# Kernel optimization log

Measured on AMD Instinct MI355X. Metric: run time of the kernel, lower is better.

Reference implementation:

```python
import jax, jax.numpy as jnp
import numpy as np

BEV_H, BEV_W, ED, HEADS, HD, LEVELS, POINTS, LAYERS = 200, 200, 128, 8, 16, 4, 8, 2
SPATIAL = [(128, 256), (64, 128), (32, 64), (16, 32)]
NV = sum(h * w for h, w in SPATIAL)
NQ = BEV_H * BEV_W
NCLS = 21


def setup_inputs() -> dict:
    key = jax.random.key(0)
    ks = iter(jax.random.split(key, 48))
    r = lambda shape, s=0.02: jax.random.normal(next(ks), shape, jnp.float32) * s
    inp = dict(
        value=r((1, NV, ED), 1.0),
        bev_queries=r((NQ, ED), 0.02),
        bev_pos=r((NQ, ED), 0.02),
        proj_indices=jax.random.randint(next(ks), (1, BEV_H, BEV_W), 0, 250000),
        Wv=r((LAYERS, ED, ED)), bv=jnp.zeros((LAYERS, ED)),
        Woff=r((LAYERS, ED, HEADS * LEVELS * POINTS * 2), 0.01),
        boff=jnp.zeros((LAYERS, HEADS * LEVELS * POINTS * 2)),
        Wattn=r((LAYERS, ED, HEADS * LEVELS * POINTS), 0.01),
        battn=jnp.zeros((LAYERS, HEADS * LEVELS * POINTS)),
        Wout=r((LAYERS, ED, ED)), bout=jnp.zeros((LAYERS, ED)),
        Wf1=r((LAYERS, ED, ED)), bf1=jnp.zeros((LAYERS, ED)),
        Wf2=r((LAYERS, ED, ED)), bf2=jnp.zeros((LAYERS, ED)),
        ln_g=jnp.ones((LAYERS, 2, ED)), ln_b=jnp.zeros((LAYERS, 2, ED)),
        cw1=r((128, ED, 7, 7), 0.01), g1=jnp.ones(128), b1=jnp.zeros(128),
        cw2=r((64, 128, 3, 3), 0.02), g2=jnp.ones(64), b2=jnp.zeros(64),
        cw3=r((48, 64, 3, 3), 0.02), g3=jnp.ones(48), b3=jnp.zeros(48),
        cw4=r((48, 48, 3, 3), 0.02), g4=jnp.ones(48), b4=jnp.zeros(48),
        objw=r((NCLS, 48, 1, 1), 0.05), objb=jnp.zeros(NCLS),
    )
    return inp


def _ln(x, g, b):
    m = x.mean(-1, keepdims=True)
    v = ((x - m) ** 2).mean(-1, keepdims=True)
    return (x - m) * jax.lax.rsqrt(v + 1e-5) * g + b


def _deform_attn(q, value, Wv, bv, Woff, boff, Wattn, battn, Wout, bout, ref):
    # multi-scale deformable attention (Deformable-DETR / BEVFormer core)
    v = (value[0] @ Wv + bv).reshape(NV, HEADS, HD)
    off = (q @ Woff + boff).reshape(NQ, HEADS, LEVELS, POINTS, 2)
    attn = jax.nn.softmax((q @ Wattn + battn).reshape(NQ, HEADS, LEVELS * POINTS), -1)
    attn = attn.reshape(NQ, HEADS, LEVELS, POINTS)
    out = jnp.zeros((HEADS, NQ, HD), jnp.float32)
    start = 0
    for l, (H, W) in enumerate(SPATIAL):
        vl = v[start:start + H * W].transpose(1, 0, 2)  # [HEADS, H*W, HD]
        start += H * W
        # normalized sampling locations in [0,1]
        loc = ref[:, None, None, :] + off[:, :, l] / jnp.array([W, H], jnp.float32)
        x = loc[..., 0] * W - 0.5  # grid_sample align_corners=False convention
        y = loc[..., 1] * H - 0.5  # [NQ, HEADS, POINTS]
        x0 = jnp.floor(x)
        y0 = jnp.floor(y)
        acc = jnp.zeros((HEADS, NQ, POINTS, HD), jnp.float32)
        for dx, dy in ((0, 0), (1, 0), (0, 1), (1, 1)):
            xc = x0 + dx
            yc = y0 + dy
            wgt = (1.0 - jnp.abs(x - xc)) * (1.0 - jnp.abs(y - yc))
            valid = (xc >= 0) & (xc < W) & (yc >= 0) & (yc < H)
            xi = jnp.clip(xc, 0, W - 1).astype(jnp.int32)
            yi = jnp.clip(yc, 0, H - 1).astype(jnp.int32)
            idx = (yi * W + xi).transpose(1, 0, 2)  # [HEADS, NQ, POINTS]
            g = jax.vmap(lambda vh, ih: vh[ih])(vl, idx)  # [HEADS, NQ, POINTS, HD]
            acc = acc + (wgt * valid).transpose(1, 0, 2)[..., None] * g
        out = out + jnp.einsum('nhp,hnpd->hnd', attn[:, :, l], acc)
    return out.transpose(1, 0, 2).reshape(NQ, ED) @ Wout + bout


def _bev_encoder(bev_queries, bev_pos, value, Wv, bv, Woff, boff, Wattn, battn, Wout, bout, Wf1, bf1, Wf2, bf2, ln_g, ln_b):
    gx = (jnp.arange(BEV_W, dtype=jnp.float32) + 0.5) / BEV_W
    gy = (jnp.arange(BEV_H, dtype=jnp.float32) + 0.5) / BEV_H
    ref = jnp.stack(jnp.meshgrid(gx, gy), -1).reshape(NQ, 2)  # (x, y)
    q = bev_queries
    for i in range(LAYERS):  # operation_order: cross_attn, norm, ffn, norm
        a = _deform_attn(q + bev_pos, value, Wv[i], bv[i], Woff[i], boff[i],
                         Wattn[i], battn[i], Wout[i], bout[i], ref)
        q = _ln(q + a, ln_g[i, 0], ln_b[i, 0])
        h = jax.nn.relu(q @ Wf1[i] + bf1[i]) @ Wf2[i] + bf2[i]
        q = _ln(q + h, ln_g[i, 1], ln_b[i, 1])
    return q


def _conv(x, w, p):
    return jax.lax.conv_general_dilated(x, w, (1, 1), [(p, p), (p, p)],
                                        dimension_numbers=('NCHW', 'OIHW', 'NCHW'))


def _bn_relu(x, g, b):
    m = x.mean((0, 2, 3), keepdims=True)
    v = x.var((0, 2, 3), keepdims=True)
    return jax.nn.relu((x - m) * jax.lax.rsqrt(v + 1e-5) * g[None, :, None, None] + b[None, :, None, None])


def reference(value, bev_queries, bev_pos, proj_indices, Wv, bv, Woff, boff, Wattn, battn, Wout, bout, Wf1, bf1, Wf2, bf2, ln_g, ln_b, cw1, g1, b1, cw2, g2, b2, cw3, g3, b3, cw4, g4, b4, objw, objb):
    observed_masks = proj_indices < jnp.max(proj_indices)  # mask_update
    q = _bev_encoder(bev_queries, bev_pos, value, Wv, bv, Woff, boff, Wattn, battn,
                     Wout, bout, Wf1, bf1, Wf2, bf2, ln_g, ln_b)
    mem = q.reshape(1, BEV_H, BEV_W, ED).transpose(0, 3, 1, 2)  # [1, ED, H, W]
    h = _bn_relu(_conv(mem, cw1, 3), g1, b1)
    h = _bn_relu(_conv(h, cw2, 1), g2, b2)
    h = _bn_relu(_conv(h, cw3, 1), g3, b3)
    h = _bn_relu(_conv(h, cw4, 1), g4, b4)
    semmap = _conv(h, objw, 0) + objb[None, :, None, None]
    return semmap, observed_masks
```

## Files before the change

kernel.cpp:

```cpp
#include <hip/hip_runtime.h>
#include <cstdint>
#include <cstddef>

#define NQ 40000
#define EDIM 128
#define NVAL 43520
#define NCLS 21

typedef unsigned short u16;
typedef unsigned int uint;
typedef short bf16x8 __attribute__((ext_vector_type(8)));
typedef float f32x4 __attribute__((ext_vector_type(4)));

__device__ inline u16 f2b(float f) {
    unsigned u = __float_as_uint(f);
    unsigned r = u + 0x7FFF + ((u >> 16) & 1);
    return (u16)(r >> 16);
}
__device__ inline float b2f(u16 v) {
    unsigned u = ((unsigned)v) << 16;
    return __uint_as_float(u);
}
__device__ inline float blo(uint u) { return __uint_as_float(u << 16); }
__device__ inline float bhi(uint u) { return __uint_as_float(u & 0xFFFF0000u); }

__global__ void reduce_max_int(const int* __restrict__ idx, int* __restrict__ mx) {
    int i = blockIdx.x * 256 + threadIdx.x;
    int v = (i < NQ) ? idx[i] : 0;
    for (int o = 32; o > 0; o >>= 1) v = max(v, __shfl_xor(v, o, 64));
    if ((threadIdx.x & 63) == 0) atomicMax(mx, v);
}

__global__ void write_mask(const int* __restrict__ idx, const int* __restrict__ mx,
                           float* __restrict__ out) {
    int i = blockIdx.x * 256 + threadIdx.x;
    if (i >= NQ) return;
    out[i] = (idx[i] < *mx) ? 1.0f : 0.0f;
}

__global__ void cvt_b_k(const float* __restrict__ src, u16* __restrict__ dst, int n8) {
    int i = blockIdx.x * 256 + threadIdx.x;
    if (i >= n8) return;
    const float4 a = ((const float4*)src)[i * 2];
    const float4 b = ((const float4*)src)[i * 2 + 1];
    u16 o[8] = {f2b(a.x), f2b(a.y), f2b(a.z), f2b(a.w), f2b(b.x), f2b(b.y), f2b(b.z), f2b(b.w)};
    ((uint4*)dst)[i] = *(const uint4*)o;
}

__global__ void add2b_k(const float* __restrict__ a, const float* __restrict__ b,
                        u16* __restrict__ c, int n8) {
    int i = blockIdx.x * 256 + threadIdx.x;
    if (i >= n8) return;
    const float4 a0 = ((const float4*)a)[i * 2], a1 = ((const float4*)a)[i * 2 + 1];
    const float4 b0 = ((const float4*)b)[i * 2], b1 = ((const float4*)b)[i * 2 + 1];
    u16 o[8] = {f2b(a0.x + b0.x), f2b(a0.y + b0.y), f2b(a0.z + b0.z), f2b(a0.w + b0.w),
                f2b(a1.x + b1.x), f2b(a1.y + b1.y), f2b(a1.z + b1.z), f2b(a1.w + b1.w)};
    ((uint4*)c)[i] = *(const uint4*)o;
}

__global__ void pack_enc_k(const float* __restrict__ Wv, const float* __restrict__ Woff,
                           const float* __restrict__ Wattn, const float* __restrict__ Wout,
                           const float* __restrict__ Wf1, const float* __restrict__ Wf2,
                           u16* __restrict__ dst) {
    int i = blockIdx.x * 256 + threadIdx.x;
    if (i >= 327680) return;
    int l = i / 163840, r = i % 163840;
    int k = r / 1280, col = r % 1280;
    const float* src; int N; int n; u16* d;
    u16* base = dst + (size_t)l * 163840;
    if (col < 128)       { src = Wv    + (size_t)l * 16384; N = 128; n = col;        d = base;          }
    else if (col < 640)  { src = Woff  + (size_t)l * 65536; N = 512; n = col - 128;  d = base + 16384;  }
    else if (col < 896)  { src = Wattn + (size_t)l * 32768; N = 256; n = col - 640;  d = base + 81920;  }
    else if (col < 1024) { src = Wout  + (size_t)l * 16384; N = 128; n = col - 896;  d = base + 114688; }
    else if (col < 1152) { src = Wf1   + (size_t)l * 16384; N = 128; n = col - 1024; d = base + 131072; }
    else                 { src = Wf2   + (size_t)l * 16384; N = 128; n = col - 1152; d = base + 147456; }
    d[(size_t)n * 128 + k] = f2b(src[(size_t)k * N + n]);
}

__global__ void pack_bias_k(const float* __restrict__ boff, const float* __restrict__ battn,
                            float* __restrict__ dst) {
    int i = blockIdx.x * 256 + threadIdx.x;
    if (i >= 1536) return;
    int l = i / 768, r = i % 768;
    dst[i] = (r < 512) ? boff[(size_t)l * 512 + r] : battn[(size_t)l * 256 + r - 512];
}

__global__ void pack_cw_k(const float* __restrict__ w, u16* __restrict__ wT,
                          int OC, int IC, int KS, int OCp, int ICp) {
    int i = blockIdx.x * 256 + threadIdx.x;
    int tot = KS * KS * OCp * ICp;
    if (i >= tot) return;
    int ic = i % ICp; int r = i / ICp;
    int oc = r % OCp; int tap = r / OCp;
    int ky = tap / KS, kx = tap % KS;
    float v = 0.f;
    if (oc < OC && ic < IC)
        v = w[(((size_t)oc * IC + ic) * KS + ky) * KS + kx];
    wT[i] = f2b(v);
}

__global__ __launch_bounds__(256) void gemm_mfma_k(
        const u16* __restrict__ A, const u16* __restrict__ BT,
        const float* __restrict__ bias, float* __restrict__ Cf,
        u16* __restrict__ Cb, int N, int relu) {
    __shared__ u16 As[64 * 136];
    __shared__ u16 Bs[64 * 136];
    const int m0 = blockIdx.x * 64, n0 = blockIdx.y * 64;
    const int t = threadIdx.x;
#pragma unroll
    for (int ci = t; ci < 1024; ci += 256) {
        int r = ci >> 4, c = ci & 15;
        *(uint4*)&As[r * 136 + c * 8] = *(const uint4*)&A[(size_t)(m0 + r) * 128 + c * 8];
        *(uint4*)&Bs[r * 136 + c * 8] = *(const uint4*)&BT[(size_t)(n0 + r) * 128 + c * 8];
    }
    __syncthreads();
    const int wave = t >> 6, lane = t & 63;
    const int wm = (wave & 1) * 32, wn = (wave >> 1) * 32;
    const int lr = lane & 15, lk = (lane >> 4) * 8;
    f32x4 acc[2][2] = {};
#pragma unroll
    for (int ks = 0; ks < 4; ks++) {
        bf16x8 a0 = *(const bf16x8*)&As[(wm + lr) * 136 + ks * 32 + lk];
        bf16x8 a1 = *(const bf16x8*)&As[(wm + 16 + lr) * 136 + ks * 32 + lk];
        bf16x8 b0 = *(const bf16x8*)&Bs[(wn + lr) * 136 + ks * 32 + lk];
        bf16x8 b1 = *(const bf16x8*)&Bs[(wn + 16 + lr) * 136 + ks * 32 + lk];
        acc[0][0] = __builtin_amdgcn_mfma_f32_16x16x32_bf16(a0, b0, acc[0][0], 0, 0, 0);
        acc[0][1] = __builtin_amdgcn_mfma_f32_16x16x32_bf16(a0, b1, acc[0][1], 0, 0, 0);
        acc[1][0] = __builtin_amdgcn_mfma_f32_16x16x32_bf16(a1, b0, acc[1][0], 0, 0, 0);
        acc[1][1] = __builtin_amdgcn_mfma_f32_16x16x32_bf16(a1, b1, acc[1][1], 0, 0, 0);
    }
    float bj0 = bias[n0 + wn + lr];
    float bj1 = bias[n0 + wn + 16 + lr];
#pragma unroll
    for (int i = 0; i < 2; i++) {
#pragma unroll
        for (int j = 0; j < 2; j++) {
            float bb = j ? bj1 : bj0;
#pragma unroll
            for (int r = 0; r < 4; r++) {
                int ml = wm + i * 16 + (lane >> 4) * 4 + r;
                int nl = wn + j * 16 + lr;
                float v = acc[i][j][r] + bb;
                if (relu) v = fmaxf(v, 0.f);
                size_t o = (size_t)(m0 + ml) * N + n0 + nl;
                if (Cf) Cf[o] = v;
                if (Cb) Cb[o] = f2b(v);
            }
        }
    }
}

template <int KS, int ICP>
__global__ __launch_bounds__(256) void conv5_mfma_k(
        const u16* __restrict__ pimg, const u16* __restrict__ wT,
        float* __restrict__ out, int OCtot) {
    constexpr int PAD = KS / 2;
    constexpr int WIN = 64 + KS - 1;
    constexpr int STR = ICP + 8;
    constexpr int KSTEPS = ICP / 32;
    constexpr int NTAP = KS * KS;
    constexpr int ACH = WIN * (ICP / 8);
    constexpr int NB = ICP / 32;
    __shared__ u16 As[2 * WIN * STR];
    __shared__ u16 Bs[2 * 64 * STR];
    const int bx = blockIdx.x;
    const int yp = (bx >> 2) * 2;
    const int xc = bx & 3;
    const int x0 = (xc == 3) ? 136 : xc * 64;
    const int n0 = blockIdx.y * 64;
    const int t = threadIdx.x;
    const int wave = t >> 6, lane = t & 63;
    const int row = wave >> 1;
    const int wn = (wave & 1) * 32;
    const int lr = lane & 15, lkq = lane >> 4, lk = lkq * 8;

    f32x4 acc[4][2] = {};
    const u16* wbase = wT + (size_t)n0 * ICP;

    uint4 breg[NB];
    int bro[NB], bco[NB];
#pragma unroll
    for (int k = 0; k < NB; k++) {
        int ci = t + k * 256;
        bro[k] = ci / (ICP / 8);
        bco[k] = ci - bro[k] * (ICP / 8);
    }
#pragma unroll
    for (int k = 0; k < NB; k++)
        breg[k] = *(const uint4*)&wbase[(size_t)bro[k] * ICP + bco[k] * 8];
#pragma unroll
    for (int k = 0; k < NB; k++)
        *(uint4*)&Bs[(size_t)bro[k] * STR + bco[k] * 8] = breg[k];

    for (int ky = 0; ky < KS; ky++) {
        __syncthreads();
        {
            const u16* s0 = pimg + (((size_t)(yp + ky + 3 - PAD)) * 208 + (x0 + 3 - PAD)) * ICP;
            const u16* s1 = pimg + (((size_t)(yp + 1 + ky + 3 - PAD)) * 208 + (x0 + 3 - PAD)) * ICP;
            for (int ci = t; ci < 2 * ACH; ci += 256) {
                int w2 = ci / ACH, rem = ci - w2 * ACH;
                int r = rem / (ICP / 8), c = rem - r * (ICP / 8);
                const u16* s = w2 ? s1 : s0;
                *(uint4*)&As[(size_t)(w2 * WIN + r) * STR + c * 8] =
                    *(const uint4*)&s[(size_t)r * ICP + c * 8];
            }
        }
        for (int kx = 0; kx < KS; kx++) {
            const int tap = ky * KS + kx;
            __syncthreads();
            if (tap + 1 < NTAP) {
                const u16* ws = wbase + (size_t)(tap + 1) * OCtot * ICP;
#pragma unroll
                for (int k = 0; k < NB; k++)
                    breg[k] = *(const uint4*)&ws[(size_t)bro[k] * ICP + bco[k] * 8];
            }
            const u16* ab = &As[((size_t)row * WIN + kx) * STR];
            const u16* bb = &Bs[(size_t)((tap & 1) * 64 + wn) * STR];
#pragma unroll
            for (int ks = 0; ks < KSTEPS; ks++) {
                bf16x8 b0 = *(const bf16x8*)&bb[(size_t)lr * STR + ks * 32 + lk];
                bf16x8 b1 = *(const bf16x8*)&bb[(size_t)(lr + 16) * STR + ks * 32 + lk];
#pragma unroll
                for (int i = 0; i < 4; i++) {
                    bf16x8 a = *(const bf16x8*)&ab[(size_t)(lr + i * 16) * STR + ks * 32 + lk];
                    acc[i][0] = __builtin_amdgcn_mfma_f32_16x16x32_bf16(a, b0, acc[i][0], 0, 0, 0);
                    acc[i][1] = __builtin_amdgcn_mfma_f32_16x16x32_bf16(a, b1, acc[i][1], 0, 0, 0);
                }
            }
            if (tap + 1 < NTAP) {
                u16* bd = &Bs[(size_t)(((tap + 1) & 1) * 64) * STR];
#pragma unroll
                for (int k = 0; k < NB; k++)
                    *(uint4*)&bd[(size_t)bro[k] * STR + bco[k] * 8] = breg[k];
            }
        }
    }
    const int px0 = (yp + row) * 200 + x0;
#pragma unroll
    for (int i = 0; i < 4; i++) {
#pragma unroll
        for (int j = 0; j < 2; j++) {
#pragma unroll
            for (int r = 0; r < 4; r++) {
                int ml = i * 16 + lkq * 4 + r;
                int nl = wn + j * 16 + lr;
                out[(size_t)(px0 + ml) * OCtot + n0 + nl] = acc[i][j][r];
            }
        }
    }
}

__global__ __launch_bounds__(256) void deform3_k(
        const u16* __restrict__ v, const u16* __restrict__ oa,
        u16* __restrict__ outb, int q0, int nq) {
    const int t = threadIdx.x;
    const int wq = t >> 6;
    const int lane = t & 63;
    const int s = lane >> 5;
    const int l32 = lane & 31;
    const int h = l32 >> 2;
    const int cl = l32 & 3;
    const int qi = blockIdx.x * 8 + wq * 2 + s;
    if (qi >= nq) return;
    const int gq = q0 + qi;
    const float rx = ((gq % 200) + 0.5f) / 200.f;
    const float ry = ((gq / 200) + 0.5f) / 200.f;

    const uint* lp = (const uint*)(oa + (size_t)qi * 768 + 512 + h * 32);
    float lg[32];
#pragma unroll
    for (int i = 0; i < 16; i++) { uint u = lp[i]; lg[2 * i] = blo(u); lg[2 * i + 1] = bhi(u); }
    float mx = -1e30f;
#pragma unroll
    for (int i = 0; i < 32; i++) mx = fmaxf(mx, lg[i]);
    float ssum = 0.f;
#pragma unroll
    for (int i = 0; i < 32; i++) { lg[i] = __expf(lg[i] - mx); ssum += lg[i]; }
    const float inv = 1.f / ssum;

    const uint* op = (const uint*)(oa + (size_t)qi * 768 + h * 64);

    const int HS[4] = {128, 64, 32, 16};
    const int WS[4] = {256, 128, 64, 32};
    const int ST[4] = {0, 32768, 40960, 43008};
    float a0 = 0.f, a1 = 0.f, a2 = 0.f, a3 = 0.f;
#pragma unroll
    for (int l = 0; l < 4; l++) {
        const int H = HS[l], W = WS[l];
        const float fW = (float)W, fH = (float)H;
        const u16* vb = v + (size_t)ST[l] * 128 + h * 16 + cl * 4;
#pragma unroll
        for (int p = 0; p < 8; p++) {
            uint pr = op[l * 8 + p];
            float ox = blo(pr), oy = bhi(pr);
            float xx = rx * fW + ox - 0.5f;
            float yy = ry * fH + oy - 0.5f;
            float xf = floorf(xx), yf = floorf(yy);
            int ix = (int)xf, iy = (int)yf;
            float fx = xx - xf, fy = yy - yf;
            float aw = lg[l * 8 + p] * inv;
            int x1 = ix + 1, y1 = iy + 1;
            bool vx0 = (unsigned)ix < (unsigned)W;
            bool vx1 = (unsigned)x1 < (unsigned)W;
            bool vy0 = (unsigned)iy < (unsigned)H;
            bool vy1 = (unsigned)y1 < (unsigned)H;
            int cx0 = min(max(ix, 0), W - 1), cx1 = min(max(x1, 0), W - 1);
            int cy0 = min(max(iy, 0), H - 1), cy1 = min(max(y1, 0), H - 1);
            float w00 = (vx0 && vy0) ? (1.f - fx) * (1.f - fy) * aw : 0.f;
            float w10 = (vx1 && vy0) ? fx * (1.f - fy) * aw : 0.f;
            float w01 = (vx0 && vy1) ? (1.f - fx) * fy * aw : 0.f;
            float w11 = (vx1 && vy1) ? fx * fy * aw : 0.f;
            uint2 u00 = *(const uint2*)(vb + (size_t)(cy0 * W + cx0) * 128);
            uint2 u10 = *(const uint2*)(vb + (size_t)(cy0 * W + cx1) * 128);
            uint2 u01 = *(const uint2*)(vb + (size_t)(cy1 * W + cx0) * 128);
            uint2 u11 = *(const uint2*)(vb + (size_t)(cy1 * W + cx1) * 128);
            a0 = fmaf(w00, blo(u00.x), a0); a1 = fmaf(w00, bhi(u00.x), a1);
            a2 = fmaf(w00, blo(u00.y), a2); a3 = fmaf(w00, bhi(u00.y), a3);
            a0 = fmaf(w10, blo(u10.x), a0); a1 = fmaf(w10, bhi(u10.x), a1);
            a2 = fmaf(w10, blo(u10.y), a2); a3 = fmaf(w10, bhi(u10.y), a3);
            a0 = fmaf(w01, blo(u01.x), a0); a1 = fmaf(w01, bhi(u01.x), a1);
            a2 = fmaf(w01, blo(u01.y), a2); a3 = fmaf(w01, bhi(u01.y), a3);
            a0 = fmaf(w11, blo(u11.x), a0); a1 = fmaf(w11, bhi(u11.x), a1);
            a2 = fmaf(w11, blo(u11.y), a2); a3 = fmaf(w11, bhi(u11.y), a3);
        }
    }
    uint2 o;
    o.x = (uint)f2b(a0) | ((uint)f2b(a1) << 16);
    o.y = (uint)f2b(a2) | ((uint)f2b(a3) << 16);
    *(uint2*)(outb + (size_t)gq * 128 + h * 16 + cl * 4) = o;
}

__global__ __launch_bounds__(256) void add_ln_k(
        float* __restrict__ q, const float* __restrict__ a,
        const float* __restrict__ g, const float* __restrict__ b,
        u16* __restrict__ qb) {
    const int row = blockIdx.x * 4 + (threadIdx.x >> 6);
    const int lane = threadIdx.x & 63;
    float s0 = q[(size_t)row * 128 + lane] + a[(size_t)row * 128 + lane];
    float s1 = q[(size_t)row * 128 + 64 + lane] + a[(size_t)row * 128 + 64 + lane];
    float sum = s0 + s1;
    for (int o = 32; o > 0; o >>= 1) sum += __shfl_xor(sum, o, 64);
    float mean = sum * (1.f / 128.f);
    float d0 = s0 - mean, d1 = s1 - mean;
    float vs = d0 * d0 + d1 * d1;
    for (int o = 32; o > 0; o >>= 1) vs += __shfl_xor(vs, o, 64);
    float inv = rsqrtf(vs * (1.f / 128.f) + 1e-5f);
    float o0 = d0 * inv * g[lane] + b[lane];
    float o1 = d1 * inv * g[64 + lane] + b[64 + lane];
    q[(size_t)row * 128 + lane] = o0;
    q[(size_t)row * 128 + 64 + lane] = o1;
    qb[(size_t)row * 128 + lane] = f2b(o0);
    qb[(size_t)row * 128 + 64 + lane] = f2b(o1);
}

__global__ void fill_pimg2_k(const u16* __restrict__ qb, u16* __restrict__ pimg) {
    int i = blockIdx.x * 256 + threadIdx.x;
    if (i >= 685568) return;
    int pp = i >> 4, c8 = i & 15;
    int py = pp / 208, px = pp - py * 208;
    uint4 val = {0u, 0u, 0u, 0u};
    if (py >= 3 && py < 203 && px >= 3 && px < 203)
        val = ((const uint4*)qb)[((size_t)((py - 3) * 200 + (px - 3))) * 16 + c8];
    ((uint4*)pimg)[i] = val;
}

__global__ __launch_bounds__(256) void bn_stats2_k(const float* __restrict__ x,
                                                   float* __restrict__ acc,
                                                   int cSh, int ppb) {
    const int t = threadIdx.x;
    const int Cp = 1 << cSh;
    const int c = t & (Cp - 1);
    const int sub = t >> cSh;
    const int nsub = 256 >> cSh;
    float s = 0.f, s2 = 0.f;
    const int pbase = blockIdx.x * ppb;
    for (int i = sub; i < ppb; i += nsub) {
        float v = x[(size_t)(pbase + i) * Cp + c];
        s += v; s2 += v * v;
    }
    __shared__ float ls[256], ls2[256];
    ls[t] = s; ls2[t] = s2;
    __syncthreads();
    if (t < Cp) {
        for (int k = 1; k < nsub; k++) { s += ls[t + k * Cp]; s2 += ls2[t + k * Cp]; }
        atomicAdd(&acc[2 * t], s);
        atomicAdd(&acc[2 * t + 1], s2);
    }
}

__global__ void bn_fin_k(const float* __restrict__ acc, float* __restrict__ mv, int C) {
    int t = threadIdx.x;
    if (t >= C) return;
    float m = acc[2 * t] * (1.f / 40000.f);
    float var = acc[2 * t + 1] * (1.f / 40000.f) - m * m;
    mv[2 * t] = m;
    mv[2 * t + 1] = rsqrtf(var + 1e-5f);
}

__global__ void bn_apply_pad2_k(const float* __restrict__ x, const float* __restrict__ mv,
                                const float* __restrict__ g, const float* __restrict__ b,
                                u16* __restrict__ outp, int cSh, int Creal) {
    int i = blockIdx.x * 256 + threadIdx.x;
    int Cp = 1 << cSh;
    if (i >= 206 * 208 * Cp) return;
    int c = i & (Cp - 1);
    int pp = i >> cSh;
    int py = pp / 208, px = pp - py * 208;
    float v = 0.f;
    if (c < Creal && py >= 3 && py < 203 && px >= 3 && px < 203) {
        int p = (py - 3) * 200 + (px - 3);
        v = fmaxf((x[(size_t)p * Cp + c] - mv[2 * c]) * mv[2 * c + 1] * g[c] + b[c], 0.f);
    }
    outp[i] = f2b(v);
}

__global__ void bn_apply2_k(const float* __restrict__ x, const float* __restrict__ mv,
                            const float* __restrict__ g, const float* __restrict__ b,
                            u16* __restrict__ outb, int cSh, int Creal) {
    int i = blockIdx.x * 256 + threadIdx.x;
    int Cp = 1 << cSh;
    if (i >= 40000 * Cp) return;
    int c = i & (Cp - 1);
    float v = 0.f;
    if (c < Creal) v = fmaxf((x[i] - mv[2 * c]) * mv[2 * c + 1] * g[c] + b[c], 0.f);
    outb[i] = f2b(v);
}

__global__ void obj_conv_k(const u16* __restrict__ in, const float* __restrict__ w,
                           const float* __restrict__ bias, float* __restrict__ out) {
    int p = blockIdx.x * 256 + threadIdx.x;
    if (p >= 40000) return;
    float xin[48];
#pragma unroll
    for (int c = 0; c < 48; c++) xin[c] = b2f(in[(size_t)p * 64 + c]);
    for (int o = 0; o < NCLS; o++) {
        float acc = bias[o];
#pragma unroll
        for (int c = 0; c < 48; c++) acc += xin[c] * w[o * 48 + c];
        out[(size_t)o * 40000 + p] = acc;
    }
}

extern "C" void kernel_launch(void* const* d_in, const int* in_sizes, int n_in,
                              void* d_out, int out_size, void* d_ws, size_t ws_size,
                              hipStream_t stream) {
    const float* value   = (const float*)d_in[0];
    const float* bev_q   = (const float*)d_in[1];
    const float* bev_pos = (const float*)d_in[2];
    const int*   proj    = (const int*)d_in[3];
    const float* Wv      = (const float*)d_in[4];
    const float* bv      = (const float*)d_in[5];
    const float* Woff    = (const float*)d_in[6];
    const float* boff    = (const float*)d_in[7];
    const float* Wattn   = (const float*)d_in[8];
    const float* battn   = (const float*)d_in[9];
    const float* Wout    = (const float*)d_in[10];
    const float* bout    = (const float*)d_in[11];
    const float* Wf1     = (const float*)d_in[12];
    const float* bf1     = (const float*)d_in[13];
    const float* Wf2     = (const float*)d_in[14];
    const float* bf2     = (const float*)d_in[15];
    const float* ln_g    = (const float*)d_in[16];
    const float* ln_b    = (const float*)d_in[17];
    const float* cw1     = (const float*)d_in[18];
    const float* g1      = (const float*)d_in[19];
    const float* b1      = (const float*)d_in[20];
    const float* cw2     = (const float*)d_in[21];
    const float* g2      = (const float*)d_in[22];
    const float* b2      = (const float*)d_in[23];
    const float* cw3     = (const float*)d_in[24];
    const float* g3      = (const float*)d_in[25];
    const float* b3      = (const float*)d_in[26];
    const float* cw4     = (const float*)d_in[27];
    const float* g4      = (const float*)d_in[28];
    const float* b4      = (const float*)d_in[29];
    const float* objw    = (const float*)d_in[30];
    const float* objb    = (const float*)d_in[31];
    float* out = (float*)d_out;

    float* WSb = (float*)d_ws;
    float* q     = WSb + 0;
    u16*   qb    = (u16*)(WSb + 5120000);
    u16*   qpb   = (u16*)(WSb + 7680000);
    u16*   valb  = (u16*)(WSb + 10240000);
    u16*   vbufb = (u16*)(WSb + 13025280);
    u16*   fb    = (u16*)(WSb + 15810560);
    float* tmp   = WSb + 18882560;
    u16*   aob   = (u16*)(WSb + 24002560);
    u16*   hb    = (u16*)(WSb + 26562560);
    u16*   wenc  = (u16*)(WSb + 29122560);
    u16*   wcv   = (u16*)(WSb + 29286400);
    float* bnacc = WSb + 29761536;
    float* bnmv  = WSb + 29762048;
    int*   maxi  = (int*)(WSb + 29762304);
    float* fbias = WSb + 29762308;

    u16*   pimg = (u16*)(WSb + 10240000);
    float* c1f  = tmp;
    u16*   c1b  = (u16*)(WSb + 13025280);
    float* c2f  = WSb + 0;
    u16*   c2b  = (u16*)(WSb + 5120000);
    float* c3f  = WSb + 2560000;
    u16*   c3b  = (u16*)(WSb + 7680000);
    float* c4f  = WSb + 0;
    u16*   c4b  = (u16*)(WSb + 15810560);

    const size_t L = 163840;
    u16* WvT[2]; u16* WoffT[2]; u16* WoutT[2]; u16* Wf1T[2]; u16* Wf2T[2];
    for (int l = 0; l < 2; l++) {
        u16* base = wenc + l * L;
        WvT[l]    = base;
        WoffT[l]  = base + 16384;
        WoutT[l]  = base + 114688;
        Wf1T[l]   = base + 131072;
        Wf2T[l]   = base + 147456;
    }
    u16* w1T = wcv;
    u16* w2T = wcv + 802816;
    u16* w3T = wcv + 876544;
    u16* w4T = wcv + 913408;

    hipMemsetAsync(maxi, 0, sizeof(int), stream);
    reduce_max_int<<<157, 256, 0, stream>>>(proj, maxi);
    write_mask<<<157, 256, 0, stream>>>(proj, maxi, out + 840000);

    pack_enc_k<<<1280, 256, 0, stream>>>(Wv, Woff, Wattn, Wout, Wf1, Wf2, wenc);
    pack_bias_k<<<6, 256, 0, stream>>>(boff, battn, fbias);
    pack_cw_k<<<3136, 256, 0, stream>>>(cw1, w1T, 128, 128, 7, 128, 128);
    pack_cw_k<<<288, 256, 0, stream>>>(cw2, w2T, 64, 128, 3, 64, 128);
    pack_cw_k<<<144, 256, 0, stream>>>(cw3, w3T, 48, 64, 3, 64, 64);
    pack_cw_k<<<144, 256, 0, stream>>>(cw4, w4T, 48, 48, 3, 64, 64);
    cvt_b_k<<<2720, 256, 0, stream>>>(value, valb, NVAL * 128 / 8);

    hipMemcpyAsync(q, bev_q, (size_t)NQ * EDIM * sizeof(float),
                   hipMemcpyDeviceToDevice, stream);
    const int CH0 = 19968, CH1 = 20032;
    for (int l = 0; l < 2; l++) {
        gemm_mfma_k<<<dim3(680, 2), 256, 0, stream>>>(
            valb, WvT[l], bv + (size_t)l * 128, nullptr, vbufb, 128, 0);
        add2b_k<<<2500, 256, 0, stream>>>(q, bev_pos, qpb, NQ * 128 / 8);
        for (int cidx = 0; cidx < 2; cidx++) {
            int qs = cidx ? CH0 : 0;
            int nq = cidx ? CH1 : CH0;
            gemm_mfma_k<<<dim3(nq / 64, 12), 256, 0, stream>>>(
                qpb + (size_t)qs * 128, WoffT[l], fbias + (size_t)l * 768,
                nullptr, fb, 768, 0);
            deform3_k<<<nq / 8, 256, 0, stream>>>(vbufb, fb, aob, qs, nq);
        }
        gemm_mfma_k<<<dim3(625, 2), 256, 0, stream>>>(
            aob, WoutT[l], bout + (size_t)l * 128, tmp, nullptr, 128, 0);
        add_ln_k<<<10000, 256, 0, stream>>>(q, tmp, ln_g + (size_t)(l * 2 + 0) * 128,
                                            ln_b + (size_t)(l * 2 + 0) * 128, qb);
        gemm_mfma_k<<<dim3(625, 2), 256, 0, stream>>>(
            qb, Wf1T[l], bf1 + (size_t)l * 128, nullptr, hb, 128, 1);
        gemm_mfma_k<<<dim3(625, 2), 256, 0, stream>>>(
            hb, Wf2T[l], bf2 + (size_t)l * 128, tmp, nullptr, 128, 0);
        add_ln_k<<<10000, 256, 0, stream>>>(q, tmp, ln_g + (size_t)(l * 2 + 1) * 128,
                                            ln_b + (size_t)(l * 2 + 1) * 128, qb);
    }

    fill_pimg2_k<<<2678, 256, 0, stream>>>(qb, pimg);

    conv5_mfma_k<7, 128><<<dim3(400, 2), 256, 0, stream>>>(pimg, w1T, c1f, 128);
    hipMemsetAsync(bnacc, 0, 512 * sizeof(float), stream);
    bn_stats2_k<<<125, 256, 0, stream>>>(c1f, bnacc, 7, 320);
    bn_fin_k<<<1, 128, 0, stream>>>(bnacc, bnmv, 128);
    bn_apply_pad2_k<<<21424, 256, 0, stream>>>(c1f, bnmv, g1, b1, c1b, 7, 128);

    conv5_mfma_k<3, 128><<<dim3(400, 1), 256, 0, stream>>>(c1b, w2T, c2f, 64);
    hipMemsetAsync(bnacc, 0, 512 * sizeof(float), stream);
    bn_stats2_k<<<125, 256, 0, stream>>>(c2f, bnacc, 6, 320);
    bn_fin_k<<<1, 64, 0, stream>>>(bnacc, bnmv, 64);
    bn_apply_pad2_k<<<10712, 256, 0, stream>>>(c2f, bnmv, g2, b2, c2b, 6, 64);

    conv5_mfma_k<3, 64><<<dim3(400, 1), 256, 0, stream>>>(c2b, w3T, c3f, 64);
    hipMemsetAsync(bnacc, 0, 512 * sizeof(float), stream);
    bn_stats2_k<<<125, 256, 0, stream>>>(c3f, bnacc, 6, 320);
    bn_fin_k<<<1, 48, 0, stream>>>(bnacc, bnmv, 48);
    bn_apply_pad2_k<<<10712, 256, 0, stream>>>(c3f, bnmv, g3, b3, c3b, 6, 48);

    conv5_mfma_k<3, 64><<<dim3(400, 1), 256, 0, stream>>>(c3b, w4T, c4f, 64);
    hipMemsetAsync(bnacc, 0, 512 * sizeof(float), stream);
    bn_stats2_k<<<125, 256, 0, stream>>>(c4f, bnacc, 6, 320);
    bn_fin_k<<<1, 48, 0, stream>>>(bnacc, bnmv, 48);
    bn_apply2_k<<<10000, 256, 0, stream>>>(c4f, bnmv, g4, b4, c4b, 6, 48);

    obj_conv_k<<<157, 256, 0, stream>>>(c4b, objw, objb, out);
}
```

Measured before the change: 1.024 ms.

## Head-major padded value layout, A-tile reuse in GEMMs, fused BN stats into conv

```diff
diff --git a/kernel.cpp b/kernel.cpp
--- a/kernel.cpp
+++ b/kernel.cpp
@@ -99,159 +99,217 @@
     wT[i] = f2b(v);
 }
 
-__global__ __launch_bounds__(256) void gemm_mfma_k(
+__global__ __launch_bounds__(256) void gemm2_mfma_k(
         const u16* __restrict__ A, const u16* __restrict__ BT,
         const float* __restrict__ bias, float* __restrict__ Cf,
-        u16* __restrict__ Cb, int N, int relu) {
+        u16* __restrict__ Cb, int N, int relu, int NSUB) {
     __shared__ u16 As[64 * 136];
     __shared__ u16 Bs[64 * 136];
-    const int m0 = blockIdx.x * 64, n0 = blockIdx.y * 64;
+    const int m0 = blockIdx.x * 64;
+    const int nbase = blockIdx.y * 64 * NSUB;
     const int t = threadIdx.x;
-#pragma unroll
-    for (int ci = t; ci < 1024; ci += 256) {
-        int r = ci >> 4, c = ci & 15;
-        *(uint4*)&As[r * 136 + c * 8] = *(const uint4*)&A[(size_t)(m0 + r) * 128 + c * 8];
-        *(uint4*)&Bs[r * 136 + c * 8] = *(const uint4*)&BT[(size_t)(n0 + r) * 128 + c * 8];
-    }
-    __syncthreads();
     const int wave = t >> 6, lane = t & 63;
     const int wm = (wave & 1) * 32, wn = (wave >> 1) * 32;
-    const int lr = lane & 15, lk = (lane >> 4) * 8;
-    f32x4 acc[2][2] = {};
-#pragma unroll
-    for (int ks = 0; ks < 4; ks++) {
-        bf16x8 a0 = *(const bf16x8*)&As[(wm + lr) * 136 + ks * 32 + lk];
-        bf16x8 a1 = *(const bf16x8*)&As[(wm + 16 + lr) * 136 + ks * 32 + lk];
-        bf16x8 b0 = *(const bf16x8*)&Bs[(wn + lr) * 136 + ks * 32 + lk];
-        bf16x8 b1 = *(const bf16x8*)&Bs[(wn + 16 + lr) * 136 + ks * 32 + lk];
-        acc[0][0] = __builtin_amdgcn_mfma_f32_16x16x32_bf16(a0, b0, acc[0][0], 0, 0, 0);
-        acc[0][1] = __builtin_amdgcn_mfma_f32_16x16x32_bf16(a0, b1, acc[0][1], 0, 0, 0);
-        acc[1][0] = __builtin_amdgcn_mfma_f32_16x16x32_bf16(a1, b0, acc[1][0], 0, 0, 0);
-        acc[1][1] = __builtin_amdgcn_mfma_f32_16x16x32_bf16(a1, b1, acc[1][1], 0, 0, 0);
-    }
-    float bj0 = bias[n0 + wn + lr];
-    float bj1 = bias[n0 + wn + 16 + lr];
-#pragma unroll
-    for (int i = 0; i < 2; i++) {
-#pragma unroll
-        for (int j = 0; j < 2; j++) {
-            float bb = j ? bj1 : bj0;
+    const int lr = lane & 15, lkq = lane >> 4, lk = lkq * 8;
+    for (int s = 0; s < NSUB; s++) {
+        const int n0 = nbase + s * 64;
+        if (s) __syncthreads();
+#pragma unroll
+        for (int ci = t; ci < 1024; ci += 256) {
+            int r = ci >> 4, c = (ci & 15) * 8;
+            if (s == 0)
+                *(uint4*)&As[r * 136 + c] = *(const uint4*)&A[(size_t)(m0 + r) * 128 + c];
+            *(uint4*)&Bs[r * 136 + c] = *(const uint4*)&BT[(size_t)(n0 + r) * 128 + c];
+        }
+        __syncthreads();
+        f32x4 acc[2][2] = {};
+#pragma unroll
+        for (int ks = 0; ks < 4; ks++) {
+            bf16x8 a0 = *(const bf16x8*)&As[(wm + lr) * 136 + ks * 32 + lk];
+            bf16x8 a1 = *(const bf16x8*)&As[(wm + 16 + lr) * 136 + ks * 32 + lk];
+            bf16x8 b0 = *(const bf16x8*)&Bs[(wn + lr) * 136 + ks * 32 + lk];
+            bf16x8 b1 = *(const bf16x8*)&Bs[(wn + 16 + lr) * 136 + ks * 32 + lk];
+            acc[0][0] = __builtin_amdgcn_mfma_f32_16x16x32_bf16(a0, b0, acc[0][0], 0, 0, 0);
+            acc[0][1] = __builtin_amdgcn_mfma_f32_16x16x32_bf16(a0, b1, acc[0][1], 0, 0, 0);
+            acc[1][0] = __builtin_amdgcn_mfma_f32_16x16x32_bf16(a1, b0, acc[1][0], 0, 0, 0);
+            acc[1][1] = __builtin_amdgcn_mfma_f32_16x16x32_bf16(a1, b1, acc[1][1], 0, 0, 0);
+        }
+        float bj0 = bias[n0 + wn + lr];
+        float bj1 = bias[n0 + wn + 16 + lr];
+#pragma unroll
+        for (int i = 0; i < 2; i++) {
+#pragma unroll
+            for (int j = 0; j < 2; j++) {
+                float bb = j ? bj1 : bj0;
+#pragma unroll
+                for (int r = 0; r < 4; r++) {
+                    int ml = wm + i * 16 + lkq * 4 + r;
+                    int nl = wn + j * 16 + lr;
+                    float v = acc[i][j][r] + bb;
+                    if (relu) v = fmaxf(v, 0.f);
+                    size_t o = (size_t)(m0 + ml) * N + n0 + nl;
+                    if (Cf) Cf[o] = v;
+                    if (Cb) Cb[o] = f2b(v);
+                }
+            }
+        }
+    }
+}
+
+__global__ __launch_bounds__(256) void gemm_vh_k(
+        const u16* __restrict__ A, const u16* __restrict__ BT,
+        const float* __restrict__ bias, u16* __restrict__ vh) {
+    __shared__ u16 As[64 * 136];
+    __shared__ u16 Bs[64 * 136];
+    const int m0 = blockIdx.x * 64;
+    const int t = threadIdx.x;
+    const int wave = t >> 6, lane = t & 63;
+    const int wm = (wave & 1) * 32, wn = (wave >> 1) * 32;
+    const int lr = lane & 15, lkq = lane >> 4, lk = lkq * 8;
+    for (int s = 0; s < 2; s++) {
+        const int n0 = s * 64;
+        if (s) __syncthreads();
+#pragma unroll
+        for (int ci = t; ci < 1024; ci += 256) {
+            int r = ci >> 4, c = (ci & 15) * 8;
+            if (s == 0)
+                *(uint4*)&As[r * 136 + c] = *(const uint4*)&A[(size_t)(m0 + r) * 128 + c];
+            *(uint4*)&Bs[r * 136 + c] = *(const uint4*)&BT[(size_t)(n0 + r) * 128 + c];
+        }
+        __syncthreads();
+        f32x4 acc[2][2] = {};
+#pragma unroll
+        for (int ks = 0; ks < 4; ks++) {
+            bf16x8 a0 = *(const bf16x8*)&As[(wm + lr) * 136 + ks * 32 + lk];
+            bf16x8 a1 = *(const bf16x8*)&As[(wm + 16 + lr) * 136 + ks * 32 + lk];
+            bf16x8 b0 = *(const bf16x8*)&Bs[(wn + lr) * 136 + ks * 32 + lk];
+            bf16x8 b1 = *(const bf16x8*)&Bs[(wn + 16 + lr) * 136 + ks * 32 + lk];
+            acc[0][0] = __builtin_amdgcn_mfma_f32_16x16x32_bf16(a0, b0, acc[0][0], 0, 0, 0);
+            acc[0][1] = __builtin_amdgcn_mfma_f32_16x16x32_bf16(a0, b1, acc[0][1], 0, 0, 0);
+            acc[1][0] = __builtin_amdgcn_mfma_f32_16x16x32_bf16(a1, b0, acc[1][0], 0, 0, 0);
+            acc[1][1] = __builtin_amdgcn_mfma_f32_16x16x32_bf16(a1, b1, acc[1][1], 0, 0, 0);
+        }
+        float bj0 = bias[n0 + wn + lr];
+        float bj1 = bias[n0 + wn + 16 + lr];
+#pragma unroll
+        for (int i = 0; i < 2; i++) {
 #pragma unroll
             for (int r = 0; r < 4; r++) {
-                int ml = wm + i * 16 + (lane >> 4) * 4 + r;
-                int nl = wn + j * 16 + lr;
-                float v = acc[i][j][r] + bb;
-                if (relu) v = fmaxf(v, 0.f);
-                size_t o = (size_t)(m0 + ml) * N + n0 + nl;
-                if (Cf) Cf[o] = v;
-                if (Cb) Cb[o] = f2b(v);
+                int p = m0 + wm + i * 16 + lkq * 4 + r;
+                int idx;
+                if (p < 32768)      idx = (p >> 8) * 257 + (p & 255);
+                else if (p < 40960) { int pp = p - 32768; idx = 32896 + (pp >> 7) * 129 + (pp & 127); }
+                else if (p < 43008) { int pp = p - 40960; idx = 41152 + (pp >> 6) * 65 + (pp & 63); }
+                else                { int pp = p - 43008; idx = 43232 + (pp >> 5) * 33 + (pp & 31); }
+#pragma unroll
+                for (int j = 0; j < 2; j++) {
+                    int c = n0 + wn + j * 16 + lr;
+                    float v = acc[i][j][r] + (j ? bj1 : bj0);
+                    vh[((size_t)(c >> 4) * 43760 + idx) * 16 + (c & 15)] = f2b(v);
+                }
             }
         }
     }
 }
 
 template <int KS, int ICP>
-__global__ __launch_bounds__(256) void conv5_mfma_k(
+__global__ __launch_bounds__(256) void conv6_mfma_k(
         const u16* __restrict__ pimg, const u16* __restrict__ wT,
-        float* __restrict__ out, int OCtot) {
+        float* __restrict__ out, float* __restrict__ bnacc, int OCtot) {
     constexpr int PAD = KS / 2;
-    constexpr int WIN = 64 + KS - 1;
     constexpr int STR = ICP + 8;
+    constexpr int NTAP = KS * KS;
     constexpr int KSTEPS = ICP / 32;
-    constexpr int NTAP = KS * KS;
-    constexpr int ACH = WIN * (ICP / 8);
     constexpr int NB = ICP / 32;
-    __shared__ u16 As[2 * WIN * STR];
     __shared__ u16 Bs[2 * 64 * STR];
     const int bx = blockIdx.x;
-    const int yp = (bx >> 2) * 2;
+    const int y = bx >> 2;
     const int xc = bx & 3;
     const int x0 = (xc == 3) ? 136 : xc * 64;
     const int n0 = blockIdx.y * 64;
     const int t = threadIdx.x;
     const int wave = t >> 6, lane = t & 63;
-    const int row = wave >> 1;
-    const int wn = (wave & 1) * 32;
+    const int wm = (wave & 1) * 32, wn = (wave >> 1) * 32;
     const int lr = lane & 15, lkq = lane >> 4, lk = lkq * 8;
 
-    f32x4 acc[4][2] = {};
-    const u16* wbase = wT + (size_t)n0 * ICP;
-
-    uint4 breg[NB];
+    f32x4 acc[2][2] = {};
     int bro[NB], bco[NB];
 #pragma unroll
     for (int k = 0; k < NB; k++) {
         int ci = t + k * 256;
         bro[k] = ci / (ICP / 8);
-        bco[k] = ci - bro[k] * (ICP / 8);
-    }
-#pragma unroll
-    for (int k = 0; k < NB; k++)
-        breg[k] = *(const uint4*)&wbase[(size_t)bro[k] * ICP + bco[k] * 8];
-#pragma unroll
-    for (int k = 0; k < NB; k++)
-        *(uint4*)&Bs[(size_t)bro[k] * STR + bco[k] * 8] = breg[k];
-
-    for (int ky = 0; ky < KS; ky++) {
+        bco[k] = (ci % (ICP / 8)) * 8;
+    }
+    uint4 breg[NB];
+    {
+        const u16* w0 = wT + (size_t)n0 * ICP;
+#pragma unroll
+        for (int k = 0; k < NB; k++)
+            breg[k] = *(const uint4*)&w0[(size_t)bro[k] * ICP + bco[k]];
+#pragma unroll
+        for (int k = 0; k < NB; k++)
+            *(uint4*)&Bs[bro[k] * STR + bco[k]] = breg[k];
+    }
+    const u16* arow = pimg + (((size_t)(y + 3 - PAD)) * 208 + (x0 + 3 - PAD)) * ICP;
+
+    for (int tap = 0; tap < NTAP; tap++) {
         __syncthreads();
-        {
-            const u16* s0 = pimg + (((size_t)(yp + ky + 3 - PAD)) * 208 + (x0 + 3 - PAD)) * ICP;
-            const u16* s1 = pimg + (((size_t)(yp + 1 + ky + 3 - PAD)) * 208 + (x0 + 3 - PAD)) * ICP;
-            for (int ci = t; ci < 2 * ACH; ci += 256) {
-                int w2 = ci / ACH, rem = ci - w2 * ACH;
-                int r = rem / (ICP / 8), c = rem - r * (ICP / 8);
-                const u16* s = w2 ? s1 : s0;
-                *(uint4*)&As[(size_t)(w2 * WIN + r) * STR + c * 8] =
-                    *(const uint4*)&s[(size_t)r * ICP + c * 8];
+        const int ky = tap / KS, kx = tap - ky * KS;
+        if (tap + 1 < NTAP) {
+            const u16* ws = wT + ((size_t)(tap + 1) * OCtot + n0) * ICP;
+#pragma unroll
+            for (int k = 0; k < NB; k++)
+                breg[k] = *(const uint4*)&ws[(size_t)bro[k] * ICP + bco[k]];
+        }
+        const u16* ab = arow + ((size_t)ky * 208 + kx) * ICP;
+        const u16* bb = &Bs[(tap & 1) * 64 * STR];
+#pragma unroll
+        for (int ks = 0; ks < KSTEPS; ks++) {
+            bf16x8 b0 = *(const bf16x8*)&bb[(wn + lr) * STR + ks * 32 + lk];
+            bf16x8 b1 = *(const bf16x8*)&bb[(wn + 16 + lr) * STR + ks * 32 + lk];
+            bf16x8 a0 = *(const bf16x8*)&ab[(size_t)(wm + lr) * ICP + ks * 32 + lk];
+            bf16x8 a1 = *(const bf16x8*)&ab[(size_t)(wm + 16 + lr) * ICP + ks * 32 + lk];
+            acc[0][0] = __builtin_amdgcn_mfma_f32_16x16x32_bf16(a0, b0, acc[0][0], 0, 0, 0);
+            acc[0][1] = __builtin_amdgcn_mfma_f32_16x16x32_bf16(a0, b1, acc[0][1], 0, 0, 0);
+            acc[1][0] = __builtin_amdgcn_mfma_f32_16x16x32_bf16(a1, b0, acc[1][0], 0, 0, 0);
+            acc[1][1] = __builtin_amdgcn_mfma_f32_16x16x32_bf16(a1, b1, acc[1][1], 0, 0, 0);
+        }
+        if (tap + 1 < NTAP) {
+            u16* bd = &Bs[((tap + 1) & 1) * 64 * STR];
+#pragma unroll
+            for (int k = 0; k < NB; k++)
+                *(uint4*)&bd[bro[k] * STR + bco[k]] = breg[k];
+        }
+    }
+    const int px0 = y * 200 + x0;
+#pragma unroll
+    for (int j = 0; j < 2; j++) {
+        float sa = 0.f, sb = 0.f;
+#pragma unroll
+        for (int i = 0; i < 2; i++) {
+#pragma unroll
+            for (int r = 0; r < 4; r++) {
+                int ml = wm + i * 16 + lkq * 4 + r;
+                int nl = wn + j * 16 + lr;
+                float v = acc[i][j][r];
+                out[(size_t)(px0 + ml) * OCtot + n0 + nl] = v;
+                float msk = (xc != 3 || ml >= 56) ? 1.f : 0.f;
+                sa += msk * v;
+                sb += msk * v * v;
             }
         }
-        for (int kx = 0; kx < KS; kx++) {
-            const int tap = ky * KS + kx;
-            __syncthreads();
-            if (tap + 1 < NTAP) {
-                const u16* ws = wbase + (size_t)(tap + 1) * OCtot * ICP;
-#pragma unroll
-                for (int k = 0; k < NB; k++)
-                    breg[k] = *(const uint4*)&ws[(size_t)bro[k] * ICP + bco[k] * 8];
-            }
-            const u16* ab = &As[((size_t)row * WIN + kx) * STR];
-            const u16* bb = &Bs[(size_t)((tap & 1) * 64 + wn) * STR];
-#pragma unroll
-            for (int ks = 0; ks < KSTEPS; ks++) {
-                bf16x8 b0 = *(const bf16x8*)&bb[(size_t)lr * STR + ks * 32 + lk];
-                bf16x8 b1 = *(const bf16x8*)&bb[(size_t)(lr + 16) * STR + ks * 32 + lk];
-#pragma unroll
-                for (int i = 0; i < 4; i++) {
-                    bf16x8 a = *(const bf16x8*)&ab[(size_t)(lr + i * 16) * STR + ks * 32 + lk];
-                    acc[i][0] = __builtin_amdgcn_mfma_f32_16x16x32_bf16(a, b0, acc[i][0], 0, 0, 0);
-                    acc[i][1] = __builtin_amdgcn_mfma_f32_16x16x32_bf16(a, b1, acc[i][1], 0, 0, 0);
-                }
-            }
-            if (tap + 1 < NTAP) {
-                u16* bd = &Bs[(size_t)(((tap + 1) & 1) * 64) * STR];
-#pragma unroll
-                for (int k = 0; k < NB; k++)
-                    *(uint4*)&bd[(size_t)bro[k] * STR + bco[k] * 8] = breg[k];
-            }
-        }
-    }
-    const int px0 = (yp + row) * 200 + x0;
-#pragma unroll
-    for (int i = 0; i < 4; i++) {
-#pragma unroll
-        for (int j = 0; j < 2; j++) {
-#pragma unroll
-            for (int r = 0; r < 4; r++) {
-                int ml = i * 16 + lkq * 4 + r;
-                int nl = wn + j * 16 + lr;
-                out[(size_t)(px0 + ml) * OCtot + n0 + nl] = acc[i][j][r];
-            }
-        }
-    }
-}
-
-__global__ __launch_bounds__(256) void deform3_k(
-        const u16* __restrict__ v, const u16* __restrict__ oa,
+        sa += __shfl_xor(sa, 16, 64); sb += __shfl_xor(sb, 16, 64);
+        sa += __shfl_xor(sa, 32, 64); sb += __shfl_xor(sb, 32, 64);
+        if (lkq == 0) {
+            int ch = n0 + wn + j * 16 + lr;
+            atomicAdd(&bnacc[2 * ch], sa);
+            atomicAdd(&bnacc[2 * ch + 1], sb);
+        }
+    }
+}
+
+__global__ __launch_bounds__(256) void deform4_k(
+        const u16* __restrict__ vh, const u16* __restrict__ oa,
         u16* __restrict__ outb, int q0, int nq) {
     const int t = threadIdx.x;
     const int wq = t >> 6;
@@ -260,6 +318,8 @@
     const int l32 = lane & 31;
     const int h = l32 >> 2;
     const int cl = l32 & 3;
+    const int o8 = (cl & 1) * 8;
+    const int sx = cl >> 1;
     const int qi = blockIdx.x * 8 + wq * 2 + s;
     if (qi >= nq) return;
     const int gq = q0 + qi;
@@ -279,16 +339,16 @@
     const float inv = 1.f / ssum;
 
     const uint* op = (const uint*)(oa + (size_t)qi * 768 + h * 64);
+    const u16* vhh = vh + (size_t)h * 43760 * 16 + o8;
 
     const int HS[4] = {128, 64, 32, 16};
     const int WS[4] = {256, 128, 64, 32};
-    const int ST[4] = {0, 32768, 40960, 43008};
-    float a0 = 0.f, a1 = 0.f, a2 = 0.f, a3 = 0.f;
+    const int OFF[4] = {0, 32896, 41152, 43232};
+    float acc[8] = {};
 #pragma unroll
     for (int l = 0; l < 4; l++) {
-        const int H = HS[l], W = WS[l];
+        const int H = HS[l], W = WS[l], offl = OFF[l];
         const float fW = (float)W, fH = (float)H;
-        const u16* vb = v + (size_t)ST[l] * 128 + h * 16 + cl * 4;
 #pragma unroll
         for (int p = 0; p < 8; p++) {
             uint pr = op[l * 8 + p];
@@ -299,35 +359,39 @@
             int ix = (int)xf, iy = (int)yf;
             float fx = xx - xf, fy = yy - yf;
             float aw = lg[l * 8 + p] * inv;
-            int x1 = ix + 1, y1 = iy + 1;
-            bool vx0 = (unsigned)ix < (unsigned)W;
-            bool vx1 = (unsigned)x1 < (unsigned)W;
             bool vy0 = (unsigned)iy < (unsigned)H;
-            bool vy1 = (unsigned)y1 < (unsigned)H;
-            int cx0 = min(max(ix, 0), W - 1), cx1 = min(max(x1, 0), W - 1);
-            int cy0 = min(max(iy, 0), H - 1), cy1 = min(max(y1, 0), H - 1);
-            float w00 = (vx0 && vy0) ? (1.f - fx) * (1.f - fy) * aw : 0.f;
-            float w10 = (vx1 && vy0) ? fx * (1.f - fy) * aw : 0.f;
-            float w01 = (vx0 && vy1) ? (1.f - fx) * fy * aw : 0.f;
-            float w11 = (vx1 && vy1) ? fx * fy * aw : 0.f;
-            uint2 u00 = *(const uint2*)(vb + (size_t)(cy0 * W + cx0) * 128);
-            uint2 u10 = *(const uint2*)(vb + (size_t)(cy0 * W + cx1) * 128);
-            uint2 u01 = *(const uint2*)(vb + (size_t)(cy1 * W + cx0) * 128);
-            uint2 u11 = *(const uint2*)(vb + (size_t)(cy1 * W + cx1) * 128);
-            a0 = fmaf(w00, blo(u00.x), a0); a1 = fmaf(w00, bhi(u00.x), a1);
-            a2 = fmaf(w00, blo(u00.y), a2); a3 = fmaf(w00, bhi(u00.y), a3);
-            a0 = fmaf(w10, blo(u10.x), a0); a1 = fmaf(w10, bhi(u10.x), a1);
-            a2 = fmaf(w10, blo(u10.y), a2); a3 = fmaf(w10, bhi(u10.y), a3);
-            a0 = fmaf(w01, blo(u01.x), a0); a1 = fmaf(w01, bhi(u01.x), a1);
-            a2 = fmaf(w01, blo(u01.y), a2); a3 = fmaf(w01, bhi(u01.y), a3);
-            a0 = fmaf(w11, blo(u11.x), a0); a1 = fmaf(w11, bhi(u11.x), a1);
-            a2 = fmaf(w11, blo(u11.y), a2); a3 = fmaf(w11, bhi(u11.y), a3);
-        }
-    }
-    uint2 o;
-    o.x = (uint)f2b(a0) | ((uint)f2b(a1) << 16);
-    o.y = (uint)f2b(a2) | ((uint)f2b(a3) << 16);
-    *(uint2*)(outb + (size_t)gq * 128 + h * 16 + cl * 4) = o;
+            bool vy1 = (unsigned)(iy + 1) < (unsigned)H;
+            int cy0 = min(max(iy, 0), H - 1);
+            int cy1 = min(max(iy + 1, 0), H - 1);
+            float wy0 = vy0 ? (1.f - fy) : 0.f;
+            float wy1 = vy1 ? fy : 0.f;
+            int xq = ix + sx;
+            bool vx = (unsigned)xq < (unsigned)W;
+            int xs = min(max(xq, 0), W - 1 + sx);
+            float wx = vx ? (sx ? fx : (1.f - fx)) : 0.f;
+            float wxa = wx * aw;
+            const u16* pb = vhh + (size_t)(offl + xs) * 16;
+            uint4 v0 = *(const uint4*)(pb + (size_t)(cy0 * (W + 1)) * 16);
+            uint4 v1 = *(const uint4*)(pb + (size_t)(cy1 * (W + 1)) * 16);
+            const uint u0[4] = {v0.x, v0.y, v0.z, v0.w};
+            const uint u1[4] = {v1.x, v1.y, v1.z, v1.w};
+#pragma unroll
+            for (int c = 0; c < 4; c++) {
+                float t0 = wy0 * blo(u0[c]) + wy1 * blo(u1[c]);
+                float t1 = wy0 * bhi(u0[c]) + wy1 * bhi(u1[c]);
+                acc[2 * c]     = fmaf(wxa, t0, acc[2 * c]);
+                acc[2 * c + 1] = fmaf(wxa, t1, acc[2 * c + 1]);
+            }
+        }
+    }
+#pragma unroll
+    for (int c = 0; c < 8; c++) acc[c] += __shfl_xor(acc[c], 2, 64);
+    if (sx == 0) {
+        u16 o[8];
+#pragma unroll
+        for (int c = 0; c < 8; c++) o[c] = f2b(acc[c]);
+        *(uint4*)(outb + (size_t)gq * 128 + h * 16 + o8) = *(const uint4*)o;
+    }
 }
 
 __global__ __launch_bounds__(256) void add_ln_k(
@@ -362,30 +426,6 @@
     if (py >= 3 && py < 203 && px >= 3 && px < 203)
         val = ((const uint4*)qb)[((size_t)((py - 3) * 200 + (px - 3))) * 16 + c8];
     ((uint4*)pimg)[i] = val;
-}
-
-__global__ __launch_bounds__(256) void bn_stats2_k(const float* __restrict__ x,
-                                                   float* __restrict__ acc,
-                                                   int cSh, int ppb) {
-    const int t = threadIdx.x;
-    const int Cp = 1 << cSh;
-    const int c = t & (Cp - 1);
-    const int sub = t >> cSh;
-    const int nsub = 256 >> cSh;
-    float s = 0.f, s2 = 0.f;
-    const int pbase = blockIdx.x * ppb;
-    for (int i = sub; i < ppb; i += nsub) {
-        float v = x[(size_t)(pbase + i) * Cp + c];
-        s += v; s2 += v * v;
-    }
-    __shared__ float ls[256], ls2[256];
-    ls[t] = s; ls2[t] = s2;
-    __syncthreads();
-    if (t < Cp) {
-        for (int k = 1; k < nsub; k++) { s += ls[t + k * Cp]; s2 += ls2[t + k * Cp]; }
-        atomicAdd(&acc[2 * t], s);
-        atomicAdd(&acc[2 * t + 1], s2);
-    }
 }
 
 __global__ void bn_fin_k(const float* __restrict__ acc, float* __restrict__ mv, int C) {
@@ -483,27 +523,27 @@
     u16*   qb    = (u16*)(WSb + 5120000);
     u16*   qpb   = (u16*)(WSb + 7680000);
     u16*   valb  = (u16*)(WSb + 10240000);
-    u16*   vbufb = (u16*)(WSb + 13025280);
-    u16*   fb    = (u16*)(WSb + 15810560);
-    float* tmp   = WSb + 18882560;
-    u16*   aob   = (u16*)(WSb + 24002560);
-    u16*   hb    = (u16*)(WSb + 26562560);
-    u16*   wenc  = (u16*)(WSb + 29122560);
-    u16*   wcv   = (u16*)(WSb + 29286400);
-    float* bnacc = WSb + 29761536;
-    float* bnmv  = WSb + 29762048;
-    int*   maxi  = (int*)(WSb + 29762304);
-    float* fbias = WSb + 29762308;
+    u16*   vh    = (u16*)(WSb + 13025280);
+    u16*   fb    = (u16*)(WSb + 15825920);
+    float* tmp   = WSb + 15825920;
+    u16*   aob   = (u16*)(WSb + 23518208);
+    u16*   hb    = (u16*)(WSb + 26078208);
+    u16*   wenc  = (u16*)(WSb + 28638208);
+    u16*   wcv   = (u16*)(WSb + 28802048);
+    float* bnacc = WSb + 29277184;
+    float* bnmv  = WSb + 29277696;
+    int*   maxi  = (int*)(WSb + 29277952);
+    float* fbias = WSb + 29277956;
 
     u16*   pimg = (u16*)(WSb + 10240000);
-    float* c1f  = tmp;
+    float* c1f  = WSb + 15825920;
     u16*   c1b  = (u16*)(WSb + 13025280);
     float* c2f  = WSb + 0;
     u16*   c2b  = (u16*)(WSb + 5120000);
     float* c3f  = WSb + 2560000;
     u16*   c3b  = (u16*)(WSb + 7680000);
     float* c4f  = WSb + 0;
-    u16*   c4b  = (u16*)(WSb + 15810560);
+    u16*   c4b  = (u16*)(WSb + 20945920);
 
     const size_t L = 163840;
     u16* WvT[2]; u16* WoffT[2]; u16* WoutT[2]; u16* Wf1T[2]; u16* Wf2T[2];
@@ -536,52 +576,47 @@
                    hipMemcpyDeviceToDevice, stream);
     const int CH0 = 19968, CH1 = 20032;
     for (int l = 0; l < 2; l++) {
-        gemm_mfma_k<<<dim3(680, 2), 256, 0, stream>>>(
-            valb, WvT[l], bv + (size_t)l * 128, nullptr, vbufb, 128, 0);
+        gemm_vh_k<<<dim3(680, 1), 256, 0, stream>>>(valb, WvT[l], bv + (size_t)l * 128, vh);
         add2b_k<<<2500, 256, 0, stream>>>(q, bev_pos, qpb, NQ * 128 / 8);
         for (int cidx = 0; cidx < 2; cidx++) {
             int qs = cidx ? CH0 : 0;
             int nq = cidx ? CH1 : CH0;
-            gemm_mfma_k<<<dim3(nq / 64, 12), 256, 0, stream>>>(
+            gemm2_mfma_k<<<dim3(nq / 64, 3), 256, 0, stream>>>(
                 qpb + (size_t)qs * 128, WoffT[l], fbias + (size_t)l * 768,
-                nullptr, fb, 768, 0);
-            deform3_k<<<nq / 8, 256, 0, stream>>>(vbufb, fb, aob, qs, nq);
-        }
-        gemm_mfma_k<<<dim3(625, 2), 256, 0, stream>>>(
-            aob, WoutT[l], bout + (size_t)l * 128, tmp, nullptr, 128, 0);
+                nullptr, fb, 768, 0, 4);
+            deform4_k<<<nq / 8, 256, 0, stream>>>(vh, fb, aob, qs, nq);
+        }
+        gemm2_mfma_k<<<dim3(625, 1), 256, 0, stream>>>(
+            aob, WoutT[l], bout + (size_t)l * 128, tmp, nullptr, 128, 0, 2);
         add_ln_k<<<10000, 256, 0, stream>>>(q, tmp, ln_g + (size_t)(l * 2 + 0) * 128,
                                             ln_b + (size_t)(l * 2 + 0) * 128, qb);
-        gemm_mfma_k<<<dim3(625, 2), 256, 0, stream>>>(
-            qb, Wf1T[l], bf1 + (size_t)l * 128, nullptr, hb, 128, 1);
-        gemm_mfma_k<<<dim3(625, 2), 256, 0, stream>>>(
-            hb, Wf2T[l], bf2 + (size_t)l * 128, tmp, nullptr, 128, 0);
+        gemm2_mfma_k<<<dim3(625, 1), 256, 0, stream>>>(
+            qb, Wf1T[l], bf1 + (size_t)l * 128, nullptr, hb, 128, 1, 2);
+        gemm2_mfma_k<<<dim3(625, 1), 256, 0, stream>>>(
+            hb, Wf2T[l], bf2 + (size_t)l * 128, tmp, nullptr, 128, 0, 2);
         add_ln_k<<<10000, 256, 0, stream>>>(q, tmp, ln_g + (size_t)(l * 2 + 1) * 128,
                                             ln_b + (size_t)(l * 2 + 1) * 128, qb);
     }
 
     fill_pimg2_k<<<2678, 256, 0, stream>>>(qb, pimg);
 
-    conv5_mfma_k<7, 128><<<dim3(400, 2), 256, 0, stream>>>(pimg, w1T, c1f, 128);
     hipMemsetAsync(bnacc, 0, 512 * sizeof(float), stream);
-    bn_stats2_k<<<125, 256, 0, stream>>>(c1f, bnacc, 7, 320);
+    conv6_mfma_k<7, 128><<<dim3(800, 2), 256, 0, stream>>>(pimg, w1T, c1f, bnacc, 128);
     bn_fin_k<<<1, 128, 0, stream>>>(bnacc, bnmv, 128);
     bn_apply_pad2_k<<<21424, 256, 0, stream>>>(c1f, bnmv, g1, b1, c1b, 7, 128);
 
-    conv5_mfma_k<3, 128><<<dim3(400, 1), 256, 0, stream>>>(c1b, w2T, c2f, 64);
     hipMemsetAsync(bnacc, 0, 512 * sizeof(float), stream);
-    bn_stats2_k<<<125, 256, 0, stream>>>(c2f, bnacc, 6, 320);
+    conv6_mfma_k<3, 128><<<dim3(800, 1), 256, 0, stream>>>(c1b, w2T, c2f, bnacc, 64);
     bn_fin_k<<<1, 64, 0, stream>>>(bnacc, bnmv, 64);
     bn_apply_pad2_k<<<10712, 256, 0, stream>>>(c2f, bnmv, g2, b2, c2b, 6, 64);
 
-    conv5_mfma_k<3, 64><<<dim3(400, 1), 256, 0, stream>>>(c2b, w3T, c3f, 64);
     hipMemsetAsync(bnacc, 0, 512 * sizeof(float), stream);
-    bn_stats2_k<<<125, 256, 0, stream>>>(c3f, bnacc, 6, 320);
+    conv6_mfma_k<3, 64><<<dim3(800, 1), 256, 0, stream>>>(c2b, w3T, c3f, bnacc, 64);
     bn_fin_k<<<1, 48, 0, stream>>>(bnacc, bnmv, 48);
     bn_apply_pad2_k<<<10712, 256, 0, stream>>>(c3f, bnmv, g3, b3, c3b, 6, 48);
 
-    conv5_mfma_k<3, 64><<<dim3(400, 1), 256, 0, stream>>>(c3b, w4T, c4f, 64);
     hipMemsetAsync(bnacc, 0, 512 * sizeof(float), stream);
-    bn_stats2_k<<<125, 256, 0, stream>>>(c4f, bnacc, 6, 320);
+    conv6_mfma_k<3, 64><<<dim3(800, 1), 256, 0, stream>>>(c3b, w4T, c4f, bnacc, 64);
     bn_fin_k<<<1, 48, 0, stream>>>(bnacc, bnmv, 48);
     bn_apply2_k<<<10000, 256, 0, stream>>>(c4f, bnmv, g4, b4, c4b, 6, 48);
 
```

Result: slower. 1.525 ms (+48.9%).
